# Kernel optimization log

Hardware: AMD Instinct MI355X
Metric: run time of the kernel (lower is better)

## Reference

```python
import jax, jax.numpy as jnp
import numpy as np

N = 100000
E = 1600000
F_IN = 256
HEADS = 8
C1 = 8
NCLS = 16
NEG_SLOPE = 0.2


def setup_inputs() -> dict:
    key = jax.random.key(0)
    ks = jax.random.split(key, 8)
    x = jax.random.normal(ks[0], (N, F_IN), dtype=jnp.float32)
    edge_index = jax.random.randint(ks[1], (2, E), 0, N, dtype=jnp.int64)
    W1 = jax.random.normal(ks[2], (F_IN, HEADS * C1), dtype=jnp.float32) * (1.0 / np.sqrt(F_IN))
    a1_src = jax.random.normal(ks[3], (HEADS, C1), dtype=jnp.float32) * 0.1
    a1_dst = jax.random.normal(ks[4], (HEADS, C1), dtype=jnp.float32) * 0.1
    b1 = jnp.zeros((HEADS * C1,), dtype=jnp.float32)
    W2 = jax.random.normal(ks[5], (HEADS * C1, NCLS), dtype=jnp.float32) * (1.0 / np.sqrt(HEADS * C1))
    a2_src = jax.random.normal(ks[6], (1, NCLS), dtype=jnp.float32) * 0.1
    a2_dst = jax.random.normal(ks[7], (1, NCLS), dtype=jnp.float32) * 0.1
    b2 = jnp.zeros((NCLS,), dtype=jnp.float32)
    return {"x": x, "edge_index": edge_index, "W1": W1, "a1_src": a1_src,
            "a1_dst": a1_dst, "b1": b1, "W2": W2, "a2_src": a2_src,
            "a2_dst": a2_dst, "b2": b2}


def gat_layer(x, src, dst, W, a_src, a_dst, b, heads, out_c, concat):
    n = x.shape[0]
    h = (x @ W).reshape(n, heads, out_c)            # [N,H,C]
    al_src = (h * a_src).sum(-1)                    # [N,H]
    al_dst = (h * a_dst).sum(-1)                    # [N,H]
    e = jax.nn.leaky_relu(al_src[src] + al_dst[dst], NEG_SLOPE)  # [E',H]
    m = jax.ops.segment_max(e, dst, num_segments=n)              # per-dst max
    alpha = jnp.exp(e - m[dst])
    denom = jax.ops.segment_sum(alpha, dst, num_segments=n)
    alpha = alpha / denom[dst]
    out = jax.ops.segment_sum(h[src] * alpha[:, :, None], dst, num_segments=n)  # [N,H,C]
    out = out.reshape(n, heads * out_c) if concat else out.mean(axis=1)
    return out + b


def reference(x, edge_index, W1, a1_src, a1_dst, b1, W2, a2_src, a2_dst, b2):
    # add self-loops (PyG GATConv default)
    loop = jnp.arange(N, dtype=edge_index.dtype)
    src = jnp.concatenate([edge_index[0], loop])
    dst = jnp.concatenate([edge_index[1], loop])
    # dropout layers are identity in eval mode
    h = jax.nn.elu(gat_layer(x, src, dst, W1, a1_src, a1_dst, b1, HEADS, C1, True))
    out = gat_layer(h, src, dst, W2, a2_src, a2_dst, b2, 1, NCLS, False)
    return jax.nn.log_softmax(out, axis=-1)
```

## Files before the change

### kernel.cpp

```cpp
#include <hip/hip_runtime.h>
#include <math.h>

#define NN   100000
#define EE   1600000
#define FIN  256
#define NCLS 16
#define NEG  0.2f

#define NEDGE (EE + NN)
#define WBKT  256
#define NBKT  ((NN + WBKT - 1) / WBKT)
#define CAP   5120
#define ABLK  4096
#define NABLK ((NEDGE + ABLK - 1) / ABLK)

#define OFF_GCNT  0
#define OFF_BASE  392
#define OFF_ROW   784
#define OFF_BKT   100788
#define OFF_ADJ   (OFF_BKT + NBKT*CAP)
#define OFF_H1B   (OFF_ADJ + NEDGE)
#define OFF_H1E   (OFF_H1B + NN*32)
#define OFF_AL1S  (OFF_H1E + NN*32)
#define OFF_AL1D  (OFF_AL1S + NN*8)
#define OFF_H2B   (OFF_AL1D + NN*8)
#define OFF_AL2S  (OFF_H2B + NN*8)
#define OFF_AL2D  (OFF_AL2S + NN)

__device__ __forceinline__ float lrelu(float x) { return x >= 0.f ? x : NEG * x; }
__device__ __forceinline__ unsigned short f2bf(float x) {
    unsigned u = __float_as_uint(x);
    return (unsigned short)((u + 0x7FFF + ((u >> 16) & 1)) >> 16);
}
__device__ __forceinline__ float bf2f(unsigned short b) {
    return __uint_as_float(((unsigned)b) << 16);
}
__device__ __forceinline__ float bflo(unsigned u) { return __uint_as_float(u << 16); }
__device__ __forceinline__ float bfhi(unsigned u) { return __uint_as_float(u & 0xFFFF0000u); }

__global__ __launch_bounds__(256) void k_binA(
    const int* __restrict__ esrc, const int* __restrict__ edst,
    int* __restrict__ gcnt, unsigned* __restrict__ bkt)
{
    __shared__ int lcnt[NBKT];
    __shared__ int lbase[NBKT];
    const int t = threadIdx.x;
    const int e0 = blockIdx.x * ABLK;
    for (int i = t; i < NBKT; i += 256) lcnt[i] = 0;
    __syncthreads();

    unsigned wrd[16];
    unsigned short bb[16], ll[16];
    #pragma unroll
    for (int j = 0; j < 16; ++j) {
        int ei = e0 + j * 256 + t;
        bb[j] = 0xFFFFu;
        if (ei < NEDGE) {
            int s, d;
            if (ei < EE) { s = esrc[ei]; d = edst[ei]; } else { s = d = ei - EE; }
            int b = d >> 8;
            wrd[j] = ((unsigned)s << 8) | (unsigned)(d & 255);
            bb[j] = (unsigned short)b;
            ll[j] = (unsigned short)atomicAdd(&lcnt[b], 1);
        }
    }
    __syncthreads();
    for (int i = t; i < NBKT; i += 256)
        lbase[i] = lcnt[i] ? atomicAdd(&gcnt[i], lcnt[i]) : 0;
    __syncthreads();
    #pragma unroll
    for (int j = 0; j < 16; ++j) {
        if (bb[j] != 0xFFFFu) {
            int b = bb[j];
            bkt[(size_t)b * CAP + lbase[b] + ll[j]] = wrd[j];
        }
    }
}

__global__ __launch_bounds__(512) void k_scanB(
    const int* __restrict__ gcnt, int* __restrict__ base, int* __restrict__ row)
{
    __shared__ int s[512];
    int t = threadIdx.x;
    int v = (t < NBKT) ? gcnt[t] : 0;
    s[t] = v;
    __syncthreads();
    for (int off = 1; off < 512; off <<= 1) {
        int u = (t >= off) ? s[t - off] : 0;
        __syncthreads();
        s[t] += u;
        __syncthreads();
    }
    if (t <= NBKT) base[t] = s[t] - v;
    if (t == 0) row[NN] = NEDGE;
}

__global__ __launch_bounds__(256) void k_binC(
    const int* __restrict__ gcnt, const int* __restrict__ base,
    const unsigned* __restrict__ bkt, int* __restrict__ row, int* __restrict__ adj)
{
    __shared__ unsigned wd[CAP];
    __shared__ int hist[256], pref[256], cnt2[256];
    const int g = blockIdx.x, t = threadIdx.x;
    const int cn = gcnt[g], bs = base[g];
    hist[t] = 0; cnt2[t] = 0;
    __syncthreads();
    for (int i = t; i < cn; i += 256) {
        unsigned w = bkt[(size_t)g * CAP + i];
        wd[i] = w;
        atomicAdd(&hist[w & 255], 1);
    }
    __syncthreads();
    int v = hist[t];
    pref[t] = v;
    __syncthreads();
    for (int off = 1; off < 256; off <<= 1) {
        int u = (t >= off) ? pref[t - off] : 0;
        __syncthreads();
        pref[t] += u;
        __syncthreads();
    }
    int ex = pref[t] - v;
    int n = g * 256 + t;
    if (n < NN) row[n] = bs + ex;
    pref[t] = ex;
    __syncthreads();
    for (int i = t; i < cn; i += 256) {
        unsigned w = wd[i];
        int dl = w & 255;
        int p = atomicAdd(&cnt2[dl], 1);
        adj[bs + pref[dl] + p] = (int)(w >> 8);
    }
}

__global__ __launch_bounds__(256) void k_gemm1(
    const float* __restrict__ x, const float* __restrict__ W1,
    const float* __restrict__ a1s, const float* __restrict__ a1d,
    unsigned short* __restrict__ h1b, float* __restrict__ al1s, float* __restrict__ al1d)
{
    __shared__ float sxT[32][68];
    __shared__ float sW[32][64];
    const int t = threadIdx.x;
    const int n0 = blockIdx.x * 64;
    const int tr = t >> 4, tc = t & 15;

    float acc[4][4] = {};

    for (int kc = 0; kc < 256; kc += 32) {
        __syncthreads();
        #pragma unroll
        for (int it = 0; it < 2; ++it) {
            int i = t + it * 256;
            int r = i >> 3, fj = i & 7;
            int n = n0 + r;
            float4 v = (n < NN) ? *(const float4*)(x + (size_t)n * FIN + kc + fj * 4)
                                : make_float4(0.f, 0.f, 0.f, 0.f);
            sxT[fj * 4 + 0][r] = v.x;
            sxT[fj * 4 + 1][r] = v.y;
            sxT[fj * 4 + 2][r] = v.z;
            sxT[fj * 4 + 3][r] = v.w;
        }
        #pragma unroll
        for (int it = 0; it < 2; ++it) {
            int i = t + it * 256;
            int r = i >> 4, fj = i & 15;
            *(float4*)&sW[r][fj * 4] = *(const float4*)(W1 + (size_t)(kc + r) * 64 + fj * 4);
        }
        __syncthreads();
        #pragma unroll
        for (int k = 0; k < 32; ++k) {
            float4 a = *(const float4*)&sxT[k][tr * 4];
            float4 b = *(const float4*)&sW[k][tc * 4];
            acc[0][0] += a.x * b.x; acc[0][1] += a.x * b.y; acc[0][2] += a.x * b.z; acc[0][3] += a.x * b.w;
            acc[1][0] += a.y * b.x; acc[1][1] += a.y * b.y; acc[1][2] += a.y * b.z; acc[1][3] += a.y * b.w;
            acc[2][0] += a.z * b.x; acc[2][1] += a.z * b.y; acc[2][2] += a.z * b.z; acc[2][3] += a.z * b.w;
            acc[3][0] += a.w * b.x; acc[3][1] += a.w * b.y; acc[3][2] += a.w * b.z; acc[3][3] += a.w * b.w;
        }
    }

    #pragma unroll
    for (int j = 0; j < 4; ++j) {
        int n = n0 + tr * 4 + j;
        if (n < NN) {
            ushort4 v = make_ushort4(f2bf(acc[j][0]), f2bf(acc[j][1]), f2bf(acc[j][2]), f2bf(acc[j][3]));
            *(ushort4*)(h1b + (size_t)n * 64 + tc * 4) = v;
        }
    }

    float sa[4], da[4];
    #pragma unroll
    for (int u = 0; u < 4; ++u) { sa[u] = a1s[tc * 4 + u]; da[u] = a1d[tc * 4 + u]; }
    #pragma unroll
    for (int j = 0; j < 4; ++j) {
        float vs = acc[j][0] * sa[0] + acc[j][1] * sa[1] + acc[j][2] * sa[2] + acc[j][3] * sa[3];
        float vd = acc[j][0] * da[0] + acc[j][1] * da[1] + acc[j][2] * da[2] + acc[j][3] * da[3];
        vs += __shfl_xor(vs, 1, 64);
        vd += __shfl_xor(vd, 1, 64);
        int n = n0 + tr * 4 + j;
        if (!(tc & 1) && n < NN) {
            al1s[n * 8 + (tc >> 1)] = vs;
            al1d[n * 8 + (tc >> 1)] = vd;
        }
    }
}

__global__ __launch_bounds__(256) void k_agg1(
    const int* __restrict__ row, const int* __restrict__ adj,
    const float* __restrict__ al1s, const float* __restrict__ al1d,
    const unsigned* __restrict__ h1b2, const float* __restrict__ b1,
    unsigned* __restrict__ h1e2)
{
    const int wv = threadIdx.x >> 6, lane = threadIdx.x & 63;
    const int n = blockIdx.x * 4 + wv;
    const int half = lane >> 5;
    const int cp   = lane & 31;
    const int h    = cp >> 2;
    const float ald = al1d[n * 8 + h];
    const int r0 = row[n], r1 = row[n + 1];

    float dsum = 0.f, ax = 0.f, ay = 0.f;
    int i = r0;
    for (; i + 3 < r1; i += 4) {
        int i0 = i + half, i1 = i + 2 + half;
        int s0 = adj[i0], s1 = adj[i1];
        float w0 = __expf(lrelu(al1s[s0 * 8 + h] + ald));
        float w1 = __expf(lrelu(al1s[s1 * 8 + h] + ald));
        unsigned u0 = h1b2[s0 * 32 + cp];
        unsigned u1 = h1b2[s1 * 32 + cp];
        dsum += w0 + w1;
        ax += w0 * bflo(u0) + w1 * bflo(u1);
        ay += w0 * bfhi(u0) + w1 * bfhi(u1);
    }
    for (; i < r1; i += 2) {
        int i0 = i + half;
        bool act = i0 < r1;
        int s0 = adj[act ? i0 : r0];
        float w0 = act ? __expf(lrelu(al1s[s0 * 8 + h] + ald)) : 0.f;
        unsigned u0 = h1b2[s0 * 32 + cp];
        dsum += w0;
        ax += w0 * bflo(u0);
        ay += w0 * bfhi(u0);
    }
    dsum += __shfl_xor(dsum, 32, 64);
    ax   += __shfl_xor(ax, 32, 64);
    ay   += __shfl_xor(ay, 32, 64);

    float inv = 1.f / dsum;
    float vx = ax * inv + b1[cp * 2];
    float vy = ay * inv + b1[cp * 2 + 1];
    vx = vx > 0.f ? vx : __expf(vx) - 1.f;
    vy = vy > 0.f ? vy : __expf(vy) - 1.f;
    if (half == 0)
        h1e2[n * 32 + cp] = (unsigned)f2bf(vx) | ((unsigned)f2bf(vy) << 16);
}

__global__ __launch_bounds__(256) void k_gemm2(
    const unsigned short* __restrict__ h1e, const float* __restrict__ W2,
    const float* __restrict__ a2s, const float* __restrict__ a2d,
    unsigned short* __restrict__ h2b, float* __restrict__ al2s, float* __restrict__ al2d)
{
    __shared__ float sW[64 * 16];
    const int t = threadIdx.x;
    for (int i = t; i < 64 * 16; i += 256) sW[i] = W2[i];
    __syncthreads();
    const int n = blockIdx.x * 16 + (t >> 4);
    const int k = t & 15;
    if (n >= NN) return;
    const unsigned short* hr = h1e + (size_t)n * 64;
    float acc = 0.f;
    #pragma unroll
    for (int c = 0; c < 64; ++c) acc += bf2f(hr[c]) * sW[c * 16 + k];
    h2b[(size_t)n * 16 + k] = f2bf(acc);
    float vs = acc * a2s[k], vd = acc * a2d[k];
    #pragma unroll
    for (int off = 1; off < 16; off <<= 1) {
        vs += __shfl_xor(vs, off, 64);
        vd += __shfl_xor(vd, off, 64);
    }
    if (k == 0) { al2s[n] = vs; al2d[n] = vd; }
}

__global__ __launch_bounds__(256) void k_agg2(
    const int* __restrict__ row, const int* __restrict__ adj,
    const float* __restrict__ al2s, const float* __restrict__ al2d,
    const unsigned* __restrict__ h2b2, const float* __restrict__ b2,
    float* __restrict__ out)
{
    const int wv = threadIdx.x >> 6, lane = threadIdx.x & 63;
    const int n = blockIdx.x * 4 + wv;
    const float ald = al2d[n];
    const int r0 = row[n], r1 = row[n + 1];

    const int j = lane >> 3;
    const int c = lane & 7;
    float dsum = 0.f, ax = 0.f, ay = 0.f;
    for (int i = r0; i < r1; i += 8) {
        int i0 = i + j;
        bool act = i0 < r1;
        int s = adj[act ? i0 : r0];
        float w = act ? __expf(lrelu(al2s[s] + ald)) : 0.f;
        unsigned u = h2b2[s * 8 + c];
        dsum += w;
        ax += w * bflo(u);
        ay += w * bfhi(u);
    }
    #pragma unroll
    for (int off = 8; off < 64; off <<= 1) {
        dsum += __shfl_xor(dsum, off, 64);
        ax   += __shfl_xor(ax, off, 64);
        ay   += __shfl_xor(ay, off, 64);
    }
    float inv = 1.f / dsum;
    float vx = ax * inv + b2[c * 2];
    float vy = ay * inv + b2[c * 2 + 1];

    float mx = fmaxf(vx, vy);
    #pragma unroll
    for (int off = 1; off < 8; off <<= 1) mx = fmaxf(mx, __shfl_xor(mx, off, 64));
    float se = __expf(vx - mx) + __expf(vy - mx);
    #pragma unroll
    for (int off = 1; off < 8; off <<= 1) se += __shfl_xor(se, off, 64);
    float ls = mx + __logf(se);
    if (j == 0)
        *(float2*)(out + (size_t)n * 16 + c * 2) = make_float2(vx - ls, vy - ls);
}

extern "C" void kernel_launch(void* const* d_in, const int* in_sizes, int n_in,
                              void* d_out, int out_size, void* d_ws, size_t ws_size,
                              hipStream_t stream)
{
    const float* x    = (const float*)d_in[0];
    const int*   eidx = (const int*)d_in[1];
    const float* W1   = (const float*)d_in[2];
    const float* a1s  = (const float*)d_in[3];
    const float* a1d  = (const float*)d_in[4];
    const float* b1   = (const float*)d_in[5];
    const float* W2   = (const float*)d_in[6];
    const float* a2s  = (const float*)d_in[7];
    const float* a2d  = (const float*)d_in[8];
    const float* b2   = (const float*)d_in[9];
    float* out = (float*)d_out;
    float* ws  = (float*)d_ws;

    const int* esrc = eidx;
    const int* edst = eidx + EE;

    int* gcnt = (int*)(ws + OFF_GCNT);
    int* base = (int*)(ws + OFF_BASE);
    int* row  = (int*)(ws + OFF_ROW);
    unsigned* bkt = (unsigned*)(ws + OFF_BKT);
    int* adj  = (int*)(ws + OFF_ADJ);
    unsigned short* h1b = (unsigned short*)(ws + OFF_H1B);
    unsigned short* h1e = (unsigned short*)(ws + OFF_H1E);
    float* al1s  = ws + OFF_AL1S;
    float* al1d  = ws + OFF_AL1D;
    unsigned short* h2b = (unsigned short*)(ws + OFF_H2B);
    float* al2s  = ws + OFF_AL2S;
    float* al2d  = ws + OFF_AL2D;

    hipMemsetAsync(gcnt, 0, 392 * sizeof(int), stream);

    k_binA <<<NABLK, 256, 0, stream>>>(esrc, edst, gcnt, bkt);
    k_scanB<<<1,     512, 0, stream>>>(gcnt, base, row);
    k_binC <<<NBKT,  256, 0, stream>>>(gcnt, base, bkt, row, adj);

    k_gemm1<<<(NN + 63) / 64, 256, 0, stream>>>(x, W1, a1s, a1d, h1b, al1s, al1d);
    k_agg1 <<<NN / 4, 256, 0, stream>>>(row, adj, al1s, al1d, (const unsigned*)h1b, b1, (unsigned*)h1e);
    k_gemm2<<<NN / 16, 256, 0, stream>>>(h1e, W2, a2s, a2d, h2b, al2s, al2d);
    k_agg2 <<<NN / 4, 256, 0, stream>>>(row, adj, al2s, al2d, (const unsigned*)h2b, b2, out);
}
```

Before: 390.0 us.

## Use bf16 MFMA for first GEMM, vectorize gemm2 loads, nontemporal bucket traffic

The first projection GEMM moves from an FP32 shared-memory tiled kernel to bf16 MFMA 16x16x32 instructions. W1 is converted to bf16 and staged in LDS, and x rows are converted on the fly. The layer-2 GEMM now reads each node's hidden row as 128-bit vectors instead of scalar shorts. Bucket writes and reads in the edge binning use nontemporal hints. The MFMA path lowers input precision to bf16 for the matmul, and every block redundantly converts all of W1.

```diff
diff --git a/kernel.cpp b/kernel.cpp
--- a/kernel.cpp
+++ b/kernel.cpp
@@ -27,6 +27,10 @@
 #define OFF_AL2S  (OFF_H2B + NN*8)
 #define OFF_AL2D  (OFF_AL2S + NN)
 
+typedef unsigned uv4 __attribute__((ext_vector_type(4)));
+using bfrag = __attribute__((ext_vector_type(8))) short;
+using ffrag = __attribute__((ext_vector_type(4))) float;
+
 __device__ __forceinline__ float lrelu(float x) { return x >= 0.f ? x : NEG * x; }
 __device__ __forceinline__ unsigned short f2bf(float x) {
     unsigned u = __float_as_uint(x);
@@ -72,7 +76,7 @@
     for (int j = 0; j < 16; ++j) {
         if (bb[j] != 0xFFFFu) {
             int b = bb[j];
-            bkt[(size_t)b * CAP + lbase[b] + ll[j]] = wrd[j];
+            __builtin_nontemporal_store(wrd[j], &bkt[(size_t)b * CAP + lbase[b] + ll[j]]);
         }
     }
 }
@@ -106,7 +110,7 @@
     hist[t] = 0; cnt2[t] = 0;
     __syncthreads();
     for (int i = t; i < cn; i += 256) {
-        unsigned w = bkt[(size_t)g * CAP + i];
+        unsigned w = __builtin_nontemporal_load(&bkt[(size_t)g * CAP + i]);
         wd[i] = w;
         atomicAdd(&hist[w & 255], 1);
     }
@@ -138,68 +142,79 @@
     const float* __restrict__ a1s, const float* __restrict__ a1d,
     unsigned short* __restrict__ h1b, float* __restrict__ al1s, float* __restrict__ al1d)
 {
-    __shared__ float sxT[32][68];
-    __shared__ float sW[32][64];
+    __shared__ short sB[8][4][64][8];
     const int t = threadIdx.x;
-    const int n0 = blockIdx.x * 64;
-    const int tr = t >> 4, tc = t & 15;
-
-    float acc[4][4] = {};
-
-    for (int kc = 0; kc < 256; kc += 32) {
-        __syncthreads();
+    for (int i = t; i < 256 * 64; i += 256) {
+        int k = i >> 6, c = i & 63;
+        sB[k >> 5][(k >> 3) & 3][c][k & 7] = (short)f2bf(W1[i]);
+    }
+    __syncthreads();
+
+    const int w = t >> 6, lane = t & 63;
+    const int m = lane & 15, q = lane >> 4;
+    const int nrow = blockIdx.x * 64 + w * 16 + m;
+    const bool rok = nrow < NN;
+    const float* xr = x + (size_t)(rok ? nrow : 0) * FIN + q * 8;
+
+    ffrag acc0 = {0.f, 0.f, 0.f, 0.f};
+    ffrag acc1 = {0.f, 0.f, 0.f, 0.f};
+    ffrag acc2 = {0.f, 0.f, 0.f, 0.f};
+    ffrag acc3 = {0.f, 0.f, 0.f, 0.f};
+
+    #pragma unroll
+    for (int kc = 0; kc < 8; ++kc) {
+        bfrag a = {0, 0, 0, 0, 0, 0, 0, 0};
+        if (rok) {
+            const float* p = xr + kc * 32;
+            float4 p0 = *(const float4*)p;
+            float4 p1 = *(const float4*)(p + 4);
+            a[0] = (short)f2bf(p0.x); a[1] = (short)f2bf(p0.y);
+            a[2] = (short)f2bf(p0.z); a[3] = (short)f2bf(p0.w);
+            a[4] = (short)f2bf(p1.x); a[5] = (short)f2bf(p1.y);
+            a[6] = (short)f2bf(p1.z); a[7] = (short)f2bf(p1.w);
+        }
+        bfrag b0 = *(const bfrag*)sB[kc][q][m];
+        bfrag b1 = *(const bfrag*)sB[kc][q][16 + m];
+        bfrag b2 = *(const bfrag*)sB[kc][q][32 + m];
+        bfrag b3 = *(const bfrag*)sB[kc][q][48 + m];
+        acc0 = __builtin_amdgcn_mfma_f32_16x16x32_bf16(a, b0, acc0, 0, 0, 0);
+        acc1 = __builtin_amdgcn_mfma_f32_16x16x32_bf16(a, b1, acc1, 0, 0, 0);
+        acc2 = __builtin_amdgcn_mfma_f32_16x16x32_bf16(a, b2, acc2, 0, 0, 0);
+        acc3 = __builtin_amdgcn_mfma_f32_16x16x32_bf16(a, b3, acc3, 0, 0, 0);
+    }
+
+    #pragma unroll
+    for (int r = 0; r < 4; ++r) {
+        int n = blockIdx.x * 64 + w * 16 + q * 4 + r;
+        if (n < NN) {
+            unsigned short* hp = h1b + (size_t)n * 64 + m;
+            hp[0]  = f2bf(acc0[r]);
+            hp[16] = f2bf(acc1[r]);
+            hp[32] = f2bf(acc2[r]);
+            hp[48] = f2bf(acc3[r]);
+        }
+    }
+
+    const float sa0 = a1s[m], sa1 = a1s[16 + m], sa2 = a1s[32 + m], sa3 = a1s[48 + m];
+    const float da0 = a1d[m], da1 = a1d[16 + m], da2 = a1d[32 + m], da3 = a1d[48 + m];
+    #pragma unroll
+    for (int r = 0; r < 4; ++r) {
+        int n = blockIdx.x * 64 + w * 16 + q * 4 + r;
+        float s0 = acc0[r] * sa0, s1 = acc1[r] * sa1, s2 = acc2[r] * sa2, s3 = acc3[r] * sa3;
+        float d0 = acc0[r] * da0, d1 = acc1[r] * da1, d2 = acc2[r] * da2, d3 = acc3[r] * da3;
         #pragma unroll
-        for (int it = 0; it < 2; ++it) {
-            int i = t + it * 256;
-            int r = i >> 3, fj = i & 7;
-            int n = n0 + r;
-            float4 v = (n < NN) ? *(const float4*)(x + (size_t)n * FIN + kc + fj * 4)
-                                : make_float4(0.f, 0.f, 0.f, 0.f);
-            sxT[fj * 4 + 0][r] = v.x;
-            sxT[fj * 4 + 1][r] = v.y;
-            sxT[fj * 4 + 2][r] = v.z;
-            sxT[fj * 4 + 3][r] = v.w;
-        }
-        #pragma unroll
-        for (int it = 0; it < 2; ++it) {
-            int i = t + it * 256;
-            int r = i >> 4, fj = i & 15;
-            *(float4*)&sW[r][fj * 4] = *(const float4*)(W1 + (size_t)(kc + r) * 64 + fj * 4);
-        }
-        __syncthreads();
-        #pragma unroll
-        for (int k = 0; k < 32; ++k) {
-            float4 a = *(const float4*)&sxT[k][tr * 4];
-            float4 b = *(const float4*)&sW[k][tc * 4];
-            acc[0][0] += a.x * b.x; acc[0][1] += a.x * b.y; acc[0][2] += a.x * b.z; acc[0][3] += a.x * b.w;
-            acc[1][0] += a.y * b.x; acc[1][1] += a.y * b.y; acc[1][2] += a.y * b.z; acc[1][3] += a.y * b.w;
-            acc[2][0] += a.z * b.x; acc[2][1] += a.z * b.y; acc[2][2] += a.z * b.z; acc[2][3] += a.z * b.w;
-            acc[3][0] += a.w * b.x; acc[3][1] += a.w * b.y; acc[3][2] += a.w * b.z; acc[3][3] += a.w * b.w;
-        }
-    }
-
-    #pragma unroll
-    for (int j = 0; j < 4; ++j) {
-        int n = n0 + tr * 4 + j;
-        if (n < NN) {
-            ushort4 v = make_ushort4(f2bf(acc[j][0]), f2bf(acc[j][1]), f2bf(acc[j][2]), f2bf(acc[j][3]));
-            *(ushort4*)(h1b + (size_t)n * 64 + tc * 4) = v;
-        }
-    }
-
-    float sa[4], da[4];
-    #pragma unroll
-    for (int u = 0; u < 4; ++u) { sa[u] = a1s[tc * 4 + u]; da[u] = a1d[tc * 4 + u]; }
-    #pragma unroll
-    for (int j = 0; j < 4; ++j) {
-        float vs = acc[j][0] * sa[0] + acc[j][1] * sa[1] + acc[j][2] * sa[2] + acc[j][3] * sa[3];
-        float vd = acc[j][0] * da[0] + acc[j][1] * da[1] + acc[j][2] * da[2] + acc[j][3] * da[3];
-        vs += __shfl_xor(vs, 1, 64);
-        vd += __shfl_xor(vd, 1, 64);
-        int n = n0 + tr * 4 + j;
-        if (!(tc & 1) && n < NN) {
-            al1s[n * 8 + (tc >> 1)] = vs;
-            al1d[n * 8 + (tc >> 1)] = vd;
+        for (int off = 1; off < 8; off <<= 1) {
+            s0 += __shfl_xor(s0, off, 64); d0 += __shfl_xor(d0, off, 64);
+            s1 += __shfl_xor(s1, off, 64); d1 += __shfl_xor(d1, off, 64);
+            s2 += __shfl_xor(s2, off, 64); d2 += __shfl_xor(d2, off, 64);
+            s3 += __shfl_xor(s3, off, 64); d3 += __shfl_xor(d3, off, 64);
+        }
+        if ((m & 7) == 0 && n < NN) {
+            int hb = m >> 3;
+            al1s[n * 8 + 0 + hb] = s0;  al1d[n * 8 + 0 + hb] = d0;
+            al1s[n * 8 + 2 + hb] = s1;  al1d[n * 8 + 2 + hb] = d1;
+            al1s[n * 8 + 4 + hb] = s2;  al1d[n * 8 + 4 + hb] = d2;
+            al1s[n * 8 + 6 + hb] = s3;  al1d[n * 8 + 6 + hb] = d3;
         }
     }
 }
@@ -255,7 +270,7 @@
 }
 
 __global__ __launch_bounds__(256) void k_gemm2(
-    const unsigned short* __restrict__ h1e, const float* __restrict__ W2,
+    const uv4* __restrict__ h1eq, const float* __restrict__ W2,
     const float* __restrict__ a2s, const float* __restrict__ a2d,
     unsigned short* __restrict__ h2b, float* __restrict__ al2s, float* __restrict__ al2d)
 {
@@ -265,11 +280,16 @@
     __syncthreads();
     const int n = blockIdx.x * 16 + (t >> 4);
     const int k = t & 15;
-    if (n >= NN) return;
-    const unsigned short* hr = h1e + (size_t)n * 64;
+    const uv4* hr = h1eq + (size_t)n * 8;
     float acc = 0.f;
     #pragma unroll
-    for (int c = 0; c < 64; ++c) acc += bf2f(hr[c]) * sW[c * 16 + k];
+    for (int q = 0; q < 8; ++q) {
+        uv4 u = hr[q];
+        acc += bflo(u.x) * sW[(q * 8 + 0) * 16 + k] + bfhi(u.x) * sW[(q * 8 + 1) * 16 + k]
+             + bflo(u.y) * sW[(q * 8 + 2) * 16 + k] + bfhi(u.y) * sW[(q * 8 + 3) * 16 + k]
+             + bflo(u.z) * sW[(q * 8 + 4) * 16 + k] + bfhi(u.z) * sW[(q * 8 + 5) * 16 + k]
+             + bflo(u.w) * sW[(q * 8 + 6) * 16 + k] + bfhi(u.w) * sW[(q * 8 + 7) * 16 + k];
+    }
     h2b[(size_t)n * 16 + k] = f2bf(acc);
     float vs = acc * a2s[k], vd = acc * a2d[k];
     #pragma unroll
@@ -351,7 +371,8 @@
     unsigned* bkt = (unsigned*)(ws + OFF_BKT);
     int* adj  = (int*)(ws + OFF_ADJ);
     unsigned short* h1b = (unsigned short*)(ws + OFF_H1B);
-    unsigned short* h1e = (unsigned short*)(ws + OFF_H1E);
+    uv4* h1eq = (uv4*)(ws + OFF_H1E);
+    unsigned* h1e2 = (unsigned*)(ws + OFF_H1E);
     float* al1s  = ws + OFF_AL1S;
     float* al1d  = ws + OFF_AL1D;
     unsigned short* h2b = (unsigned short*)(ws + OFF_H2B);
@@ -365,7 +386,7 @@
     k_binC <<<NBKT,  256, 0, stream>>>(gcnt, base, bkt, row, adj);
 
     k_gemm1<<<(NN + 63) / 64, 256, 0, stream>>>(x, W1, a1s, a1d, h1b, al1s, al1d);
-    k_agg1 <<<NN / 4, 256, 0, stream>>>(row, adj, al1s, al1d, (const unsigned*)h1b, b1, (unsigned*)h1e);
-    k_gemm2<<<NN / 16, 256, 0, stream>>>(h1e, W2, a2s, a2d, h2b, al2s, al2d);
+    k_agg1 <<<NN / 4, 256, 0, stream>>>(row, adj, al1s, al1d, (const unsigned*)h1b, b1, h1e2);
+    k_gemm2<<<NN / 16, 256, 0, stream>>>(h1eq, W2, a2s, a2d, h2b, al2s, al2d);
     k_agg2 <<<NN / 4, 256, 0, stream>>>(row, adj, al2s, al2d, (const unsigned*)h2b, b2, out);
 }
```

Result: slower. 419.0 us (+7.4%).
